# Performance work log

Hardware: AMD Instinct MI355X
Metric: run time of the kernel (lower is better)

## Reference

```python
import jax, jax.numpy as jnp
import numpy as np

D = 64   # hidden dim (input_dim == hidden_dims[i] == 64)
L = 6    # GNN layers per NBFNet
EPS = 1e-5

def _layer_norm(x, g, b):
    m = jnp.mean(x, axis=-1, keepdims=True)
    v = jnp.var(x, axis=-1, keepdims=True)
    return (x - m) * jax.lax.rsqrt(v + EPS) * g + b

def _conv(x, boundary, relation, edge_index, edge_type, W, b, g, bt):
    # GeneralizedRelationalConv: distmult message, sum aggregation with
    # boundary self-loop message, linear([input, agg]) -> LayerNorm -> ReLU.
    src, dst = edge_index[0], edge_index[1]
    msg = x[:, src, :] * relation[:, edge_type, :]                # [B,E,D]
    agg = boundary + jnp.zeros_like(x).at[:, dst, :].add(msg)     # edge_weight == 1
    out = jnp.einsum('bnf,fo->bno', jnp.concatenate([x, agg], axis=-1), W) + b
    return jax.nn.relu(_layer_norm(out, g, bt))

def _rel_model(q_rel, rel_edge_index, rel_edge_type, num_rel_nodes,
               rel_emb, Wr, br, gr, btr):
    # RelNBFNet.bellmanford: query = ones, boundary scatter at query relation node.
    B = q_rel.shape[0]
    query = jnp.ones((B, D), dtype=rel_emb.dtype)
    boundary = jnp.zeros((B, num_rel_nodes, D), rel_emb.dtype).at[jnp.arange(B), q_rel].add(query)
    relation = jnp.broadcast_to(rel_emb[None], (B,) + rel_emb.shape)  # dependent=False embedding
    def step(x, p):
        W, b, g, bt = p
        h = _conv(x, boundary, relation, rel_edge_index, rel_edge_type, W, b, g, bt)
        return h + x, None  # short_cut residual
    x, _ = jax.lax.scan(step, boundary, (Wr, br, gr, btr))
    return x  # [B, R, D]  (concat_hidden=False -> hiddens[-1])

def _ent_model(rel_repr, h_index, r_index, t_index, edge_index, edge_type,
               num_nodes, Wp1, bp1, Wp2, bp2, We, be, ge, bte, W1, b1, W2, b2):
    B = h_index.shape[0]
    query = rel_repr[jnp.arange(B), r_index]                      # [B,D]
    boundary = jnp.zeros((B, num_nodes, D), query.dtype).at[jnp.arange(B), h_index].add(query)
    def step(x, p):
        wp1, b1p, wp2, b2p, W, b, g, bt = p
        # project_relations=True: per-layer 2-layer MLP on relation representations
        rel = jax.nn.relu(rel_repr @ wp1 + b1p) @ wp2 + b2p       # [B,R,D]
        h = _conv(x, boundary, rel, edge_index, edge_type, W, b, g, bt)
        return h + x, None
    x, _ = jax.lax.scan(step, boundary, (Wp1, bp1, Wp2, bp2, We, be, ge, bte))
    node_query = jnp.broadcast_to(query[:, None, :], x.shape)
    feat = jnp.concatenate([x, node_query], axis=-1)              # [B,N,2D]
    feat = feat[jnp.arange(B)[:, None], t_index]                  # gather tails [B,K,2D]
    h = jax.nn.relu(feat @ W1 + b1)                               # num_mlp_layers=2
    return (h @ W2 + b2)[..., 0]                                  # [B,K]

def setup_inputs() -> dict:
    key = jax.random.key(0)
    ks = jax.random.split(key, 16)
    B, K, N, E, R, Er = 4, 256, 20000, 200000, 200, 4000
    ND = 100  # direct relations; R = 2*ND
    h = jax.random.randint(ks[0], (B,), 0, N)
    r = jax.random.randint(ks[1], (B,), 0, ND)
    t = jax.random.randint(ks[2], (B, K), 0, N)
    batch = jnp.stack([jnp.broadcast_to(h[:, None], (B, K)), t,
                       jnp.broadcast_to(r[:, None], (B, K))], axis=-1)
    s = 0.05
    return dict(
        batch=batch,
        edge_index=jax.random.randint(ks[3], (2, E), 0, N),
        edge_type=jax.random.randint(ks[4], (E,), 0, R),
        rel_edge_index=jax.random.randint(ks[5], (2, Er), 0, R),
        rel_edge_type=jax.random.randint(ks[6], (Er,), 0, 4),
        num_nodes=N, num_rel_nodes=R,
        rel_emb=jax.random.normal(ks[7], (4, D)) * s,
        Wr=jax.random.normal(ks[8], (L, 2 * D, D)) * s,
        br=jnp.zeros((L, D)), gr=jnp.ones((L, D)), btr=jnp.zeros((L, D)),
        Wp1=jax.random.normal(ks[9], (L, D, D)) * s,
        bp1=jnp.zeros((L, D)),
        Wp2=jax.random.normal(ks[10], (L, D, D)) * s,
        bp2=jnp.zeros((L, D)),
        We=jax.random.normal(ks[11], (L, 2 * D, D)) * s,
        be=jnp.zeros((L, D)), ge=jnp.ones((L, D)), bte=jnp.zeros((L, D)),
        W1=jax.random.normal(ks[12], (2 * D, 2 * D)) * s,
        b1=jnp.zeros((2 * D,)),
        W2=jax.random.normal(ks[13], (2 * D, 1)) * s,
        b2=jnp.zeros((1,)),
    )

def reference(batch, edge_index, edge_type, rel_edge_index, rel_edge_type,
              num_nodes, num_rel_nodes,
              rel_emb, Wr, br, gr, btr,
              Wp1, bp1, Wp2, bp2, We, be, ge, bte, W1, b1, W2, b2):
    # batch holds tail-negative triples (h, t, r) with constant h and r per row,
    # so negative_sample_to_tail is the identity here (eval mode: no edge removal).
    h_index = batch[:, 0, 0]
    t_index = batch[:, :, 1]
    r_index = batch[:, 0, 2]
    rel_repr = _rel_model(r_index, rel_edge_index, rel_edge_type, num_rel_nodes,
                          rel_emb, Wr, br, gr, btr)
    return _ent_model(rel_repr, h_index, r_index, t_index, edge_index, edge_type,
                      num_nodes, Wp1, bp1, Wp2, bp2, We, be, ge, bte, W1, b1, W2, b2)
```

## Files before the change

kernel.cpp:

```cpp
#include <hip/hip_runtime.h>
#include <hip/hip_bf16.h>

#define D_   64
#define L_   6
#define B_   4
#define K_   256
#define NN   20000
#define EE   200000
#define RR   200
#define ER_  4000
#define EPS_ 1e-5f

typedef unsigned short u16;
typedef unsigned int   u32;
typedef short bf16x8 __attribute__((ext_vector_type(8)));
typedef float f32x4  __attribute__((ext_vector_type(4)));

__device__ __forceinline__ u16 f2bf(float f) {
    u32 u = __float_as_uint(f);
    u += 0x7FFF + ((u >> 16) & 1);
    return (u16)(u >> 16);
}
__device__ __forceinline__ u32 pack2bf(float a, float b) {
    return (u32)f2bf(a) | ((u32)f2bf(b) << 16);
}
__device__ __forceinline__ float bflo(u32 u) { return __uint_as_float(u << 16); }
__device__ __forceinline__ float bfhi(u32 u) { return __uint_as_float(u & 0xFFFF0000u); }

__global__ __launch_bounds__(256)
void k_zero2(int* __restrict__ ec, int* __restrict__ rc) {
    int i = blockIdx.x * 256 + threadIdx.x;
    if (i < NN) ec[i] = 0;
    else if (i < NN + RR) rc[i - NN] = 0;
}

__global__ __launch_bounds__(256)
void k_hist2(const int* __restrict__ ei, const int* __restrict__ rei,
             int* __restrict__ ec, int* __restrict__ rc) {
    int g = blockIdx.x * 256 + threadIdx.x;
    if (g < EE) atomicAdd(&ec[ei[EE + g]], 1);
    else if (g < EE + ER_) atomicAdd(&rc[rei[ER_ + (g - EE)]], 1);
}

__global__ __launch_bounds__(256)
void k_scan1_2(const int* __restrict__ e_counts, int* __restrict__ e_pre, int* __restrict__ e_bs,
               const int* __restrict__ r_counts, int* __restrict__ r_pre, int* __restrict__ r_bs,
               int ent_nb) {
    __shared__ int tsum[256];
    const int* counts; int* pre; int* bs; int n; int blk;
    if ((int)blockIdx.x < ent_nb) { counts = e_counts; pre = e_pre; bs = e_bs; n = NN; blk = blockIdx.x; }
    else                          { counts = r_counts; pre = r_pre; bs = r_bs; n = RR; blk = 0; }
    int tid = threadIdx.x;
    int base = blk * 1024 + tid * 4;
    int c0 = 0, c1 = 0, c2 = 0, c3 = 0;
    if (base + 0 < n) c0 = counts[base + 0];
    if (base + 1 < n) c1 = counts[base + 1];
    if (base + 2 < n) c2 = counts[base + 2];
    if (base + 3 < n) c3 = counts[base + 3];
    tsum[tid] = c0 + c1 + c2 + c3;
    __syncthreads();
    if (tid == 0) {
        int acc = 0;
        for (int i = 0; i < 256; i++) { int t = tsum[i]; tsum[i] = acc; acc += t; }
    }
    __syncthreads();
    int run = tsum[tid];
    if (base + 0 < n) pre[base + 0] = run; run += c0;
    if (base + 1 < n) pre[base + 1] = run; run += c1;
    if (base + 2 < n) pre[base + 2] = run; run += c2;
    if (base + 3 < n) pre[base + 3] = run; run += c3;
    if (tid == 255) bs[blk] = run;
}

__global__ __launch_bounds__(64)
void k_scan2_2(int* __restrict__ eb, int enb, int* __restrict__ etot,
               int* __restrict__ rb, int rnb, int* __restrict__ rtot) {
    if (threadIdx.x == 0) {
        int acc = 0;
        for (int i = 0; i < enb; i++) { int t = eb[i]; eb[i] = acc; acc += t; }
        *etot = acc;
    }
    if (threadIdx.x == 1) {
        int acc = 0;
        for (int i = 0; i < rnb; i++) { int t = rb[i]; rb[i] = acc; acc += t; }
        *rtot = acc;
    }
}

__global__ __launch_bounds__(256)
void k_scan3_2(int* __restrict__ e_rp, const int* __restrict__ e_bs, int* __restrict__ e_cur,
               int* __restrict__ r_rp, const int* __restrict__ r_bs, int* __restrict__ r_cur) {
    int i = blockIdx.x * 256 + threadIdx.x;
    if (i < NN) {
        int v = e_rp[i] + e_bs[i >> 10];
        e_rp[i] = v; e_cur[i] = v;
    } else if (i < NN + RR) {
        int j = i - NN;
        int v = r_rp[j] + r_bs[j >> 10];
        r_rp[j] = v; r_cur[j] = v;
    }
}

__global__ __launch_bounds__(256)
void k_fill2(const int* __restrict__ ei, const int* __restrict__ et,
             const int* __restrict__ rei, const int* __restrict__ ret,
             int* __restrict__ e_cur, int* __restrict__ r_cur,
             int* __restrict__ e_packed, int* __restrict__ r_packed) {
    int g = blockIdx.x * 256 + threadIdx.x;
    if (g < EE) {
        int pos = atomicAdd(&e_cur[ei[EE + g]], 1);
        e_packed[pos] = ei[g] | (et[g] << 15);
    } else if (g < EE + ER_) {
        int h = g - EE;
        int pos = atomicAdd(&r_cur[rei[ER_ + h]], 1);
        r_packed[pos] = rei[h] | (ret[h] << 15);
    }
}

template<int NNODES, int MODE, bool FIRST>
__global__ __launch_bounds__(256)
void k_layer9(const float* __restrict__ xin, float* __restrict__ xout,
              const u16* __restrict__ xbin, u16* __restrict__ xbout,
              const void* __restrict__ relv,
              const int* __restrict__ rowptr, const int* __restrict__ packed,
              const float* __restrict__ query, const int* __restrict__ batch,
              const float* __restrict__ W, const float* __restrict__ bias,
              const float* __restrict__ gw, const float* __restrict__ bt) {
    __shared__ u16 Wt[64][72];
    __shared__ u16 As[16][72];
    __shared__ u16 Xs[16][72];
    __shared__ float LNbuf[16][68];
    const int tid   = threadIdx.x;
    const int node0 = blockIdx.x * 4;
    const int lane  = tid & 63;
    const int wv    = tid >> 6;

    int bn0 = batch[0 * K_ * 3 + (MODE ? 0 : 2)];
    int bn1 = batch[1 * K_ * 3 + (MODE ? 0 : 2)];
    int bn2 = batch[2 * K_ * 3 + (MODE ? 0 : 2)];
    int bn3 = batch[3 * K_ * 3 + (MODE ? 0 : 2)];

    const int gnode = node0 + wv;
    int beg = 0, end = 0;
    if (gnode < NNODES) { beg = rowptr[gnode]; end = rowptr[gnode + 1]; }

    const int erow  = wv * 4 + (lane >> 4);
    const int tx    = lane & 15;
    float4 resf = make_float4(0.f, 0.f, 0.f, 0.f);
    if constexpr (!FIRST) {
        int b = erow >> 2, nd = node0 + (erow & 3);
        if (nd < NNODES)
            resf = *reinterpret_cast<const float4*>(
                xin + ((size_t)b * NNODES + nd) * 64 + tx * 4);
    }

    {
        int n = lane, k16 = wv * 16;
        u32 buf[8];
        #pragma unroll
        for (int j2 = 0; j2 < 8; j2++) {
            float w0 = W[(64 + k16 + 2 * j2    ) * 64 + n];
            float w1 = W[(64 + k16 + 2 * j2 + 1) * 64 + n];
            buf[j2] = pack2bf(w0, w1);
        }
        uint4* dst = reinterpret_cast<uint4*>(&Wt[n][k16]);
        dst[0] = make_uint4(buf[0], buf[1], buf[2], buf[3]);
        dst[1] = make_uint4(buf[4], buf[5], buf[6], buf[7]);
    }

    if (tid < 128) {
        int m = tid >> 3, o8 = (tid & 7) * 8;
        int b = m >> 2, node = node0 + (m & 3);
        uint4 v = make_uint4(0, 0, 0, 0);
        if (node < NNODES) {
            if constexpr (FIRST) {
                int bnb = (b==0)?bn0:(b==1)?bn1:(b==2)?bn2:bn3;
                if (node == bnb) {
                    if constexpr (MODE == 1) {
                        const float* q = query + b * 64 + o8;
                        v = make_uint4(pack2bf(q[0], q[1]), pack2bf(q[2], q[3]),
                                       pack2bf(q[4], q[5]), pack2bf(q[6], q[7]));
                    } else {
                        v = make_uint4(0x3F803F80u, 0x3F803F80u, 0x3F803F80u, 0x3F803F80u);
                    }
                }
            } else if constexpr (MODE == 1) {
                v = *reinterpret_cast<const uint4*>(
                    xbin + ((size_t)b * NNODES + node) * 64 + o8);
            } else {
                const float* src = xin + ((size_t)b * NNODES + node) * 64 + o8;
                float4 x0 = *reinterpret_cast<const float4*>(src);
                float4 x1 = *reinterpret_cast<const float4*>(src + 4);
                v = make_uint4(pack2bf(x0.x, x0.y), pack2bf(x0.z, x0.w),
                               pack2bf(x1.x, x1.y), pack2bf(x1.z, x1.w));
            }
        }
        *reinterpret_cast<uint4*>(&Xs[m][o8]) = v;
    }

    const int slot = lane >> 3;
    const int d8   = lane & 7;

    float qreg[4][8];
    if constexpr (MODE == 1) {
        #pragma unroll
        for (int b = 0; b < 4; b++) {
            float4 q0 = *reinterpret_cast<const float4*>(query + b * 64 + d8 * 8);
            float4 q1 = *reinterpret_cast<const float4*>(query + b * 64 + d8 * 8 + 4);
            qreg[b][0]=q0.x; qreg[b][1]=q0.y; qreg[b][2]=q0.z; qreg[b][3]=q0.w;
            qreg[b][4]=q1.x; qreg[b][5]=q1.y; qreg[b][6]=q1.z; qreg[b][7]=q1.w;
        }
    }

    {
        float acc[4][8];
        #pragma unroll
        for (int b = 0; b < 4; b++)
            #pragma unroll
            for (int i = 0; i < 8; i++) acc[b][i] = 0.f;

        for (int e0 = beg; e0 < end; e0 += 16) {
            #pragma unroll
            for (int half = 0; half < 2; half++) {
                int e = e0 + half * 8 + slot;
                if (e < end) {
                    int p = packed[e];
                    int src = p & 0x7FFF;
                    int et  = p >> 15;
                    if constexpr (MODE == 1) {
                        const u16* rb = (const u16*)relv;
                        if constexpr (FIRST) {
                            #pragma unroll
                            for (int b = 0; b < 4; b++) {
                                int bnb = (b==0)?bn0:(b==1)?bn1:(b==2)?bn2:bn3;
                                if (src == bnb) {
                                    uint4 rv = *reinterpret_cast<const uint4*>(
                                        rb + ((size_t)(b * RR + et)) * 64 + d8 * 8);
                                    acc[b][0] = fmaf(qreg[b][0], bflo(rv.x), acc[b][0]);
                                    acc[b][1] = fmaf(qreg[b][1], bfhi(rv.x), acc[b][1]);
                                    acc[b][2] = fmaf(qreg[b][2], bflo(rv.y), acc[b][2]);
                                    acc[b][3] = fmaf(qreg[b][3], bfhi(rv.y), acc[b][3]);
                                    acc[b][4] = fmaf(qreg[b][4], bflo(rv.z), acc[b][4]);
                                    acc[b][5] = fmaf(qreg[b][5], bfhi(rv.z), acc[b][5]);
                                    acc[b][6] = fmaf(qreg[b][6], bflo(rv.w), acc[b][6]);
                                    acc[b][7] = fmaf(qreg[b][7], bfhi(rv.w), acc[b][7]);
                                }
                            }
                        } else {
                            #pragma unroll
                            for (int b = 0; b < 4; b++) {
                                uint4 xv = *reinterpret_cast<const uint4*>(
                                    xbin + ((size_t)(b * NNODES + src)) * 64 + d8 * 8);
                                uint4 rv = *reinterpret_cast<const uint4*>(
                                    ((const u16*)relv) + ((size_t)(b * RR + et)) * 64 + d8 * 8);
                                acc[b][0] = fmaf(bflo(xv.x), bflo(rv.x), acc[b][0]);
                                acc[b][1] = fmaf(bfhi(xv.x), bfhi(rv.x), acc[b][1]);
                                acc[b][2] = fmaf(bflo(xv.y), bflo(rv.y), acc[b][2]);
                                acc[b][3] = fmaf(bfhi(xv.y), bfhi(rv.y), acc[b][3]);
                                acc[b][4] = fmaf(bflo(xv.z), bflo(rv.z), acc[b][4]);
                                acc[b][5] = fmaf(bfhi(xv.z), bfhi(rv.z), acc[b][5]);
                                acc[b][6] = fmaf(bflo(xv.w), bflo(rv.w), acc[b][6]);
                                acc[b][7] = fmaf(bfhi(xv.w), bfhi(rv.w), acc[b][7]);
                            }
                        }
                    } else {
                        const float* re = (const float*)relv;
                        if constexpr (FIRST) {
                            bool m0 = (src == bn0), m1 = (src == bn1),
                                 m2 = (src == bn2), m3 = (src == bn3);
                            if (m0 | m1 | m2 | m3) {
                                float4 r0 = *reinterpret_cast<const float4*>(re + et * 64 + d8 * 8);
                                float4 r1 = *reinterpret_cast<const float4*>(re + et * 64 + d8 * 8 + 4);
                                float rr[8] = {r0.x,r0.y,r0.z,r0.w,r1.x,r1.y,r1.z,r1.w};
                                if (m0) {
                                    #pragma unroll
                                    for (int i = 0; i < 8; i++) acc[0][i] += rr[i];
                                }
                                if (m1) {
                                    #pragma unroll
                                    for (int i = 0; i < 8; i++) acc[1][i] += rr[i];
                                }
                                if (m2) {
                                    #pragma unroll
                                    for (int i = 0; i < 8; i++) acc[2][i] += rr[i];
                                }
                                if (m3) {
                                    #pragma unroll
                                    for (int i = 0; i < 8; i++) acc[3][i] += rr[i];
                                }
                            }
                        } else {
                            float4 r0 = *reinterpret_cast<const float4*>(re + et * 64 + d8 * 8);
                            float4 r1 = *reinterpret_cast<const float4*>(re + et * 64 + d8 * 8 + 4);
                            #pragma unroll
                            for (int b = 0; b < 4; b++) {
                                const float* xr = xin + ((size_t)(b * NNODES + src)) * 64 + d8 * 8;
                                float4 x0 = *reinterpret_cast<const float4*>(xr);
                                float4 x1 = *reinterpret_cast<const float4*>(xr + 4);
                                acc[b][0] = fmaf(x0.x, r0.x, acc[b][0]);
                                acc[b][1] = fmaf(x0.y, r0.y, acc[b][1]);
                                acc[b][2] = fmaf(x0.z, r0.z, acc[b][2]);
                                acc[b][3] = fmaf(x0.w, r0.w, acc[b][3]);
                                acc[b][4] = fmaf(x1.x, r1.x, acc[b][4]);
                                acc[b][5] = fmaf(x1.y, r1.y, acc[b][5]);
                                acc[b][6] = fmaf(x1.z, r1.z, acc[b][6]);
                                acc[b][7] = fmaf(x1.w, r1.w, acc[b][7]);
                            }
                        }
                    }
                }
            }
        }

        #pragma unroll
        for (int b = 0; b < 4; b++)
            #pragma unroll
            for (int i = 0; i < 8; i++) {
                float v = acc[b][i];
                v += __shfl_xor(v, 8);
                v += __shfl_xor(v, 16);
                v += __shfl_xor(v, 32);
                acc[b][i] = v;
            }

        if (slot < 4) {
            float out[8];
            #pragma unroll
            for (int i = 0; i < 8; i++)
                out[i] = (slot==0) ? acc[0][i] : (slot==1) ? acc[1][i]
                       : (slot==2) ? acc[2][i] : acc[3][i];
            int bnb = (slot==0)?bn0:(slot==1)?bn1:(slot==2)?bn2:bn3;
            if (gnode < NNODES && gnode == bnb) {
                if constexpr (MODE == 1) {
                    #pragma unroll
                    for (int i = 0; i < 8; i++)
                        out[i] += (slot==0)?qreg[0][i]:(slot==1)?qreg[1][i]
                                 :(slot==2)?qreg[2][i]:qreg[3][i];
                } else {
                    #pragma unroll
                    for (int i = 0; i < 8; i++) out[i] += 1.0f;
                }
            }
            int m = slot * 4 + wv;
            *reinterpret_cast<uint4*>(&As[m][d8 * 8]) =
                make_uint4(pack2bf(out[0], out[1]), pack2bf(out[2], out[3]),
                           pack2bf(out[4], out[5]), pack2bf(out[6], out[7]));
        }
    }
    __syncthreads();

    const int al = lane & 15;
    const int ag = lane >> 4;
    const int nt = wv;
    f32x4 acc4 = (f32x4){0.f, 0.f, 0.f, 0.f};
    {
        bf16x8 a0 = *reinterpret_cast<const bf16x8*>(&As[al][ag * 8]);
        bf16x8 a1 = *reinterpret_cast<const bf16x8*>(&As[al][32 + ag * 8]);
        bf16x8 b0 = *reinterpret_cast<const bf16x8*>(&Wt[nt * 16 + al][ag * 8]);
        bf16x8 b1 = *reinterpret_cast<const bf16x8*>(&Wt[nt * 16 + al][32 + ag * 8]);
        acc4 = __builtin_amdgcn_mfma_f32_16x16x32_bf16(a0, b0, acc4, 0, 0, 0);
        acc4 = __builtin_amdgcn_mfma_f32_16x16x32_bf16(a1, b1, acc4, 0, 0, 0);
    }
    __syncthreads();

    {
        int n = lane, k16 = wv * 16;
        u32 buf[8];
        #pragma unroll
        for (int j2 = 0; j2 < 8; j2++) {
            float w0 = W[(k16 + 2 * j2    ) * 64 + n];
            float w1 = W[(k16 + 2 * j2 + 1) * 64 + n];
            buf[j2] = pack2bf(w0, w1);
        }
        uint4* dst = reinterpret_cast<uint4*>(&Wt[n][k16]);
        dst[0] = make_uint4(buf[0], buf[1], buf[2], buf[3]);
        dst[1] = make_uint4(buf[4], buf[5], buf[6], buf[7]);
    }
    __syncthreads();

    {
        bf16x8 x0 = *reinterpret_cast<const bf16x8*>(&Xs[al][ag * 8]);
        bf16x8 x1 = *reinterpret_cast<const bf16x8*>(&Xs[al][32 + ag * 8]);
        bf16x8 b0 = *reinterpret_cast<const bf16x8*>(&Wt[nt * 16 + al][ag * 8]);
        bf16x8 b1 = *reinterpret_cast<const bf16x8*>(&Wt[nt * 16 + al][32 + ag * 8]);
        acc4 = __builtin_amdgcn_mfma_f32_16x16x32_bf16(x0, b0, acc4, 0, 0, 0);
        acc4 = __builtin_amdgcn_mfma_f32_16x16x32_bf16(x1, b1, acc4, 0, 0, 0);
    }
    #pragma unroll
    for (int reg = 0; reg < 4; reg++)
        LNbuf[ag * 4 + reg][nt * 16 + al] = acc4[reg];
    __syncthreads();

    {
        int row = erow;
        int b = row >> 2, node = node0 + (row & 3);
        float o[4];
        float s1 = 0.f, s2 = 0.f;
        #pragma unroll
        for (int i = 0; i < 4; i++) {
            o[i] = LNbuf[row][tx * 4 + i] + bias[tx * 4 + i];
            s1 += o[i];
            s2 += o[i] * o[i];
        }
        s1 += __shfl_xor(s1, 1); s2 += __shfl_xor(s2, 1);
        s1 += __shfl_xor(s1, 2); s2 += __shfl_xor(s2, 2);
        s1 += __shfl_xor(s1, 4); s2 += __shfl_xor(s2, 4);
        s1 += __shfl_xor(s1, 8); s2 += __shfl_xor(s2, 8);
        float mean = s1 * (1.f / 64.f);
        float var  = s2 * (1.f / 64.f) - mean * mean;
        float inv  = rsqrtf(var + EPS_);
        if (node < NNODES) {
            int bnb = (b==0)?bn0:(b==1)?bn1:(b==2)?bn2:bn3;
            size_t ro = ((size_t)b * NNODES + node) * 64;
            float r[4] = {resf.x, resf.y, resf.z, resf.w};
            if constexpr (FIRST) {
                r[0] = r[1] = r[2] = r[3] = 0.f;
                if (node == bnb) {
                    if constexpr (MODE == 1) {
                        float4 q = *reinterpret_cast<const float4*>(query + b * 64 + tx * 4);
                        r[0] = q.x; r[1] = q.y; r[2] = q.z; r[3] = q.w;
                    } else {
                        r[0] = r[1] = r[2] = r[3] = 1.0f;
                    }
                }
            }
            float nv[4];
            #pragma unroll
            for (int i = 0; i < 4; i++) {
                float h = (o[i] - mean) * inv * gw[tx * 4 + i] + bt[tx * 4 + i];
                h = fmaxf(h, 0.f);
                nv[i] = r[i] + h;
            }
            *reinterpret_cast<float4*>(&xout[ro + tx * 4]) =
                make_float4(nv[0], nv[1], nv[2], nv[3]);
            if constexpr (MODE == 1) {
                ushort4 b4;
                b4.x = f2bf(nv[0]); b4.y = f2bf(nv[1]);
                b4.z = f2bf(nv[2]); b4.w = f2bf(nv[3]);
                *reinterpret_cast<ushort4*>(&xbout[ro + tx * 4]) = b4;
            }
        }
    }
}

__global__ __launch_bounds__(64)
void k_rel_mlp_all(const float* __restrict__ rel_repr,
                   const float* __restrict__ Wp1, const float* __restrict__ bp1,
                   const float* __restrict__ Wp2, const float* __restrict__ bp2,
                   u16* __restrict__ out) {
    __shared__ float rowv[64];
    __shared__ float hid[64];
    int l     = blockIdx.x / (B_ * RR);
    int rowid = blockIdx.x % (B_ * RR);
    int d = threadIdx.x;
    const float* w1 = Wp1 + l * 4096;
    const float* w2 = Wp2 + l * 4096;
    rowv[d] = rel_repr[rowid * 64 + d];
    __syncthreads();
    float acc = bp1[l * 64 + d];
    for (int k = 0; k < 64; k++) acc = fmaf(rowv[k], w1[k * 64 + d], acc);
    hid[d] = fmaxf(acc, 0.f);
    __syncthreads();
    float o = bp2[l * 64 + d];
    for (int k = 0; k < 64; k++) o = fmaf(hid[k], w2[k * 64 + d], o);
    out[(size_t)l * B_ * RR * 64 + rowid * 64 + d] = f2bf(o);
}

__global__ __launch_bounds__(256)
void k_query(const float* __restrict__ rel_repr, const int* __restrict__ batch,
             float* __restrict__ query) {
    int tid = threadIdx.x;
    int b = tid >> 6;
    int d = tid & 63;
    int r = batch[b * K_ * 3 + 2];
    query[b * 64 + d] = rel_repr[(b * RR + r) * 64 + d];
}

__global__ __launch_bounds__(128)
void k_final(const float* __restrict__ x, const float* __restrict__ query,
             const int* __restrict__ batch,
             const float* __restrict__ W1, const float* __restrict__ b1,
             const float* __restrict__ W2, const float* __restrict__ b2,
             float* __restrict__ out) {
    __shared__ float feat[128];
    __shared__ float partial[2];
    int pair = blockIdx.x;
    int b = pair / K_;
    int t = batch[pair * 3 + 1];
    int d = threadIdx.x;
    feat[d] = (d < 64) ? x[(size_t)(b * NN + t) * 64 + d] : query[b * 64 + (d - 64)];
    __syncthreads();
    float h = b1[d];
    for (int i = 0; i < 128; i++) h = fmaf(feat[i], W1[i * 128 + d], h);
    h = fmaxf(h, 0.f);
    float v = h * W2[d];
    #pragma unroll
    for (int off = 1; off < 64; off <<= 1) v += __shfl_xor(v, off);
    if ((d & 63) == 0) partial[d >> 6] = v;
    __syncthreads();
    if (d == 0) out[pair] = partial[0] + partial[1] + b2[0];
}

extern "C" void kernel_launch(void* const* d_in, const int* in_sizes, int n_in,
                              void* d_out, int out_size, void* d_ws, size_t ws_size,
                              hipStream_t stream) {
    const int* batch      = (const int*)d_in[0];
    const int* edge_index = (const int*)d_in[1];
    const int* edge_type  = (const int*)d_in[2];
    const int* rel_ei     = (const int*)d_in[3];
    const int* rel_et     = (const int*)d_in[4];
    const float* rel_emb = (const float*)d_in[7];
    const float* Wr  = (const float*)d_in[8];
    const float* br  = (const float*)d_in[9];
    const float* gr  = (const float*)d_in[10];
    const float* btr = (const float*)d_in[11];
    const float* Wp1 = (const float*)d_in[12];
    const float* bp1 = (const float*)d_in[13];
    const float* Wp2 = (const float*)d_in[14];
    const float* bp2 = (const float*)d_in[15];
    const float* We  = (const float*)d_in[16];
    const float* be  = (const float*)d_in[17];
    const float* ge  = (const float*)d_in[18];
    const float* bte = (const float*)d_in[19];
    const float* W1  = (const float*)d_in[20];
    const float* b1  = (const float*)d_in[21];
    const float* W2  = (const float*)d_in[22];
    const float* b2  = (const float*)d_in[23];

    float* ws = (float*)d_ws;
    float* rel_buf0 = ws;
    float* rel_buf1 = rel_buf0 + 51200;
    float* query    = rel_buf1 + 51200;
    float* x0       = query + 256;
    float* x1       = x0 + (size_t)B_ * NN * 64;
    u16*   xb0      = (u16*)(x1 + (size_t)B_ * NN * 64);
    u16*   xb1      = xb0 + (size_t)B_ * NN * 64;
    u16*   rel_all  = xb1 + (size_t)B_ * NN * 64;
    int*   iw       = (int*)(rel_all + (size_t)L_ * B_ * RR * 64);

    int* ent_counts  = iw;
    int* ent_rowptr  = ent_counts + NN;
    int* ent_bsums   = ent_rowptr + NN + 1;
    int* ent_packed  = ent_bsums + 32;
    int* rel_counts  = ent_packed + EE;
    int* rel_rowptr  = rel_counts + RR;
    int* rel_bsums   = rel_rowptr + RR + 1;
    int* rel_packed  = rel_bsums + 8;

    const int ENT_NB = (NN + 1023) / 1024;
    const int REL_NB = (RR + 1023) / 1024;

    k_zero2<<<(NN + RR + 255) / 256, 256, 0, stream>>>(ent_counts, rel_counts);
    k_hist2<<<(EE + ER_ + 255) / 256, 256, 0, stream>>>(edge_index, rel_ei, ent_counts, rel_counts);
    k_scan1_2<<<ENT_NB + REL_NB, 256, 0, stream>>>(ent_counts, ent_rowptr, ent_bsums,
                                                   rel_counts, rel_rowptr, rel_bsums, ENT_NB);
    k_scan2_2<<<1, 64, 0, stream>>>(ent_bsums, ENT_NB, ent_rowptr + NN,
                                    rel_bsums, REL_NB, rel_rowptr + RR);
    k_scan3_2<<<(NN + RR + 255) / 256, 256, 0, stream>>>(ent_rowptr, ent_bsums, ent_counts,
                                                         rel_rowptr, rel_bsums, rel_counts);
    k_fill2<<<(EE + ER_ + 255) / 256, 256, 0, stream>>>(edge_index, edge_type, rel_ei, rel_et,
                                                        ent_counts, rel_counts, ent_packed, rel_packed);

    float* rf[2] = {rel_buf0, rel_buf1};
    const int RGRID = (RR + 3) / 4;
    k_layer9<RR, 0, true><<<RGRID, 256, 0, stream>>>(
        nullptr, rf[0], nullptr, nullptr, rel_emb,
        rel_rowptr, rel_packed, nullptr, batch,
        Wr, br, gr, btr);
    int rc = 0;
    for (int l = 1; l < L_; ++l) {
        k_layer9<RR, 0, false><<<RGRID, 256, 0, stream>>>(
            rf[rc], rf[rc ^ 1], nullptr, nullptr, rel_emb,
            rel_rowptr, rel_packed, nullptr, batch,
            Wr + l * 8192, br + l * 64, gr + l * 64, btr + l * 64);
        rc ^= 1;
    }
    float* rel_final = rf[rc];

    k_query<<<1, 256, 0, stream>>>(rel_final, batch, query);
    k_rel_mlp_all<<<L_ * B_ * RR, 64, 0, stream>>>(rel_final, Wp1, bp1, Wp2, bp2, rel_all);
    float* xf[2] = {x0, x1};
    u16*   xh[2] = {xb0, xb1};
    const int EGRID = (NN + 3) / 4;
    k_layer9<NN, 1, true><<<EGRID, 256, 0, stream>>>(
        nullptr, xf[0], nullptr, xh[0], rel_all,
        ent_rowptr, ent_packed, query, batch,
        We, be, ge, bte);
    int ec = 0;
    for (int l = 1; l < L_; ++l) {
        k_layer9<NN, 1, false><<<EGRID, 256, 0, stream>>>(
            xf[ec], xf[ec ^ 1], xh[ec], xh[ec ^ 1],
            rel_all + (size_t)l * B_ * RR * 64,
            ent_rowptr, ent_packed, query, batch,
            We + l * 8192, be + l * 64, ge + l * 64, bte + l * 64);
        ec ^= 1;
    }
    k_final<<<B_ * K_, 128, 0, stream>>>(xf[ec], query, batch, W1, b1, W2, b2,
                                         (float*)d_out);
}
```

Baseline: 400.7 us.

## Make layer kernel persistent with grid-stride tiles and hoisted bf16 weights

The layer kernel becomes persistent: each block converts and stages both halves of the 128x64 weight matrix in LDS once, then loops over 4-node tiles in grid-stride fashion. The entity layers launch a fixed 1536 blocks instead of one block per tile, and launch bounds request 6 blocks per CU. This removes the per-tile global weight reload, bf16 conversion and the extra barriers between the two GEMM halves. In exchange it uses more LDS per block, may lower occupancy or constrain registers, and can leave load imbalance across the fixed grid.

Measured after the change: 692.0 us. 1.73x slower.

```diff
diff --git a/kernel.cpp b/kernel.cpp
--- a/kernel.cpp
+++ b/kernel.cpp
@@ -118,20 +118,20 @@
 }
 
 template<int NNODES, int MODE, bool FIRST>
-__global__ __launch_bounds__(256)
-void k_layer9(const float* __restrict__ xin, float* __restrict__ xout,
-              const u16* __restrict__ xbin, u16* __restrict__ xbout,
-              const void* __restrict__ relv,
-              const int* __restrict__ rowptr, const int* __restrict__ packed,
-              const float* __restrict__ query, const int* __restrict__ batch,
-              const float* __restrict__ W, const float* __restrict__ bias,
-              const float* __restrict__ gw, const float* __restrict__ bt) {
-    __shared__ u16 Wt[64][72];
+__global__ __launch_bounds__(256, 6)
+void k_layer10(const float* __restrict__ xin, float* __restrict__ xout,
+               const u16* __restrict__ xbin, u16* __restrict__ xbout,
+               const void* __restrict__ relv,
+               const int* __restrict__ rowptr, const int* __restrict__ packed,
+               const float* __restrict__ query, const int* __restrict__ batch,
+               const float* __restrict__ W, const float* __restrict__ bias,
+               const float* __restrict__ gw, const float* __restrict__ bt,
+               int ntiles) {
+    __shared__ u16 Wt[2][64][72];
     __shared__ u16 As[16][72];
     __shared__ u16 Xs[16][72];
-    __shared__ float LNbuf[16][68];
+    __shared__ float LNbuf[16][65];
     const int tid   = threadIdx.x;
-    const int node0 = blockIdx.x * 4;
     const int lane  = tid & 63;
     const int wv    = tid >> 6;
 
@@ -140,68 +140,24 @@
     int bn2 = batch[2 * K_ * 3 + (MODE ? 0 : 2)];
     int bn3 = batch[3 * K_ * 3 + (MODE ? 0 : 2)];
 
-    const int gnode = node0 + wv;
-    int beg = 0, end = 0;
-    if (gnode < NNODES) { beg = rowptr[gnode]; end = rowptr[gnode + 1]; }
-
-    const int erow  = wv * 4 + (lane >> 4);
-    const int tx    = lane & 15;
-    float4 resf = make_float4(0.f, 0.f, 0.f, 0.f);
-    if constexpr (!FIRST) {
-        int b = erow >> 2, nd = node0 + (erow & 3);
-        if (nd < NNODES)
-            resf = *reinterpret_cast<const float4*>(
-                xin + ((size_t)b * NNODES + nd) * 64 + tx * 4);
-    }
-
-    {
+    #pragma unroll
+    for (int half = 0; half < 2; half++) {
         int n = lane, k16 = wv * 16;
         u32 buf[8];
         #pragma unroll
         for (int j2 = 0; j2 < 8; j2++) {
-            float w0 = W[(64 + k16 + 2 * j2    ) * 64 + n];
-            float w1 = W[(64 + k16 + 2 * j2 + 1) * 64 + n];
+            float w0 = W[(half * 64 + k16 + 2 * j2    ) * 64 + n];
+            float w1 = W[(half * 64 + k16 + 2 * j2 + 1) * 64 + n];
             buf[j2] = pack2bf(w0, w1);
         }
-        uint4* dst = reinterpret_cast<uint4*>(&Wt[n][k16]);
+        uint4* dst = reinterpret_cast<uint4*>(&Wt[half][n][k16]);
         dst[0] = make_uint4(buf[0], buf[1], buf[2], buf[3]);
         dst[1] = make_uint4(buf[4], buf[5], buf[6], buf[7]);
     }
 
-    if (tid < 128) {
-        int m = tid >> 3, o8 = (tid & 7) * 8;
-        int b = m >> 2, node = node0 + (m & 3);
-        uint4 v = make_uint4(0, 0, 0, 0);
-        if (node < NNODES) {
-            if constexpr (FIRST) {
-                int bnb = (b==0)?bn0:(b==1)?bn1:(b==2)?bn2:bn3;
-                if (node == bnb) {
-                    if constexpr (MODE == 1) {
-                        const float* q = query + b * 64 + o8;
-                        v = make_uint4(pack2bf(q[0], q[1]), pack2bf(q[2], q[3]),
-                                       pack2bf(q[4], q[5]), pack2bf(q[6], q[7]));
-                    } else {
-                        v = make_uint4(0x3F803F80u, 0x3F803F80u, 0x3F803F80u, 0x3F803F80u);
-                    }
-                }
-            } else if constexpr (MODE == 1) {
-                v = *reinterpret_cast<const uint4*>(
-                    xbin + ((size_t)b * NNODES + node) * 64 + o8);
-            } else {
-                const float* src = xin + ((size_t)b * NNODES + node) * 64 + o8;
-                float4 x0 = *reinterpret_cast<const float4*>(src);
-                float4 x1 = *reinterpret_cast<const float4*>(src + 4);
-                v = make_uint4(pack2bf(x0.x, x0.y), pack2bf(x0.z, x0.w),
-                               pack2bf(x1.x, x1.y), pack2bf(x1.z, x1.w));
-            }
-        }
-        *reinterpret_cast<uint4*>(&Xs[m][o8]) = v;
-    }
-
+    float qreg[4][8];
     const int slot = lane >> 3;
     const int d8   = lane & 7;
-
-    float qreg[4][8];
     if constexpr (MODE == 1) {
         #pragma unroll
         for (int b = 0; b < 4; b++) {
@@ -212,232 +168,262 @@
         }
     }
 
-    {
-        float acc[4][8];
-        #pragma unroll
-        for (int b = 0; b < 4; b++)
+    const int erow = wv * 4 + (lane >> 4);
+    const int tx   = lane & 15;
+    const int al   = lane & 15;
+    const int ag   = lane >> 4;
+
+    for (int tile = blockIdx.x; tile < ntiles; tile += gridDim.x) {
+        const int node0 = tile * 4;
+
+        const int gnode = node0 + wv;
+        int beg = 0, end = 0;
+        if (gnode < NNODES) { beg = rowptr[gnode]; end = rowptr[gnode + 1]; }
+
+        float4 resf = make_float4(0.f, 0.f, 0.f, 0.f);
+        if constexpr (!FIRST) {
+            int b = erow >> 2, nd = node0 + (erow & 3);
+            if (nd < NNODES)
+                resf = *reinterpret_cast<const float4*>(
+                    xin + ((size_t)b * NNODES + nd) * 64 + tx * 4);
+        }
+
+        if (tid < 128) {
+            int m = tid >> 3, o8 = (tid & 7) * 8;
+            int b = m >> 2, node = node0 + (m & 3);
+            uint4 v = make_uint4(0, 0, 0, 0);
+            if (node < NNODES) {
+                if constexpr (FIRST) {
+                    int bnb = (b==0)?bn0:(b==1)?bn1:(b==2)?bn2:bn3;
+                    if (node == bnb) {
+                        if constexpr (MODE == 1) {
+                            const float* q = query + b * 64 + o8;
+                            v = make_uint4(pack2bf(q[0], q[1]), pack2bf(q[2], q[3]),
+                                           pack2bf(q[4], q[5]), pack2bf(q[6], q[7]));
+                        } else {
+                            v = make_uint4(0x3F803F80u, 0x3F803F80u, 0x3F803F80u, 0x3F803F80u);
+                        }
+                    }
+                } else if constexpr (MODE == 1) {
+                    v = *reinterpret_cast<const uint4*>(
+                        xbin + ((size_t)b * NNODES + node) * 64 + o8);
+                } else {
+                    const float* src = xin + ((size_t)b * NNODES + node) * 64 + o8;
+                    float4 x0 = *reinterpret_cast<const float4*>(src);
+                    float4 x1 = *reinterpret_cast<const float4*>(src + 4);
+                    v = make_uint4(pack2bf(x0.x, x0.y), pack2bf(x0.z, x0.w),
+                                   pack2bf(x1.x, x1.y), pack2bf(x1.z, x1.w));
+                }
+            }
+            *reinterpret_cast<uint4*>(&Xs[m][o8]) = v;
+        }
+
+        {
+            float acc[4][8];
             #pragma unroll
-            for (int i = 0; i < 8; i++) acc[b][i] = 0.f;
-
-        for (int e0 = beg; e0 < end; e0 += 16) {
-            #pragma unroll
-            for (int half = 0; half < 2; half++) {
-                int e = e0 + half * 8 + slot;
-                if (e < end) {
-                    int p = packed[e];
-                    int src = p & 0x7FFF;
-                    int et  = p >> 15;
-                    if constexpr (MODE == 1) {
-                        const u16* rb = (const u16*)relv;
-                        if constexpr (FIRST) {
-                            #pragma unroll
-                            for (int b = 0; b < 4; b++) {
-                                int bnb = (b==0)?bn0:(b==1)?bn1:(b==2)?bn2:bn3;
-                                if (src == bnb) {
+            for (int b = 0; b < 4; b++)
+                #pragma unroll
+                for (int i = 0; i < 8; i++) acc[b][i] = 0.f;
+
+            for (int e0 = beg; e0 < end; e0 += 16) {
+                #pragma unroll
+                for (int half = 0; half < 2; half++) {
+                    int e = e0 + half * 8 + slot;
+                    if (e < end) {
+                        int p = packed[e];
+                        int src = p & 0x7FFF;
+                        int et  = p >> 15;
+                        if constexpr (MODE == 1) {
+                            const u16* rb = (const u16*)relv;
+                            if constexpr (FIRST) {
+                                #pragma unroll
+                                for (int b = 0; b < 4; b++) {
+                                    int bnb = (b==0)?bn0:(b==1)?bn1:(b==2)?bn2:bn3;
+                                    if (src == bnb) {
+                                        uint4 rv = *reinterpret_cast<const uint4*>(
+                                            rb + ((size_t)(b * RR + et)) * 64 + d8 * 8);
+                                        acc[b][0] = fmaf(qreg[b][0], bflo(rv.x), acc[b][0]);
+                                        acc[b][1] = fmaf(qreg[b][1], bfhi(rv.x), acc[b][1]);
+                                        acc[b][2] = fmaf(qreg[b][2], bflo(rv.y), acc[b][2]);
+                                        acc[b][3] = fmaf(qreg[b][3], bfhi(rv.y), acc[b][3]);
+                                        acc[b][4] = fmaf(qreg[b][4], bflo(rv.z), acc[b][4]);
+                                        acc[b][5] = fmaf(qreg[b][5], bfhi(rv.z), acc[b][5]);
+                                        acc[b][6] = fmaf(qreg[b][6], bflo(rv.w), acc[b][6]);
+                                        acc[b][7] = fmaf(qreg[b][7], bfhi(rv.w), acc[b][7]);
+                                    }
+                                }
+                            } else {
+                                #pragma unroll
+                                for (int b = 0; b < 4; b++) {
+                                    uint4 xv = *reinterpret_cast<const uint4*>(
+                                        xbin + ((size_t)(b * NNODES + src)) * 64 + d8 * 8);
                                     uint4 rv = *reinterpret_cast<const uint4*>(
-                                        rb + ((size_t)(b * RR + et)) * 64 + d8 * 8);
-                                    acc[b][0] = fmaf(qreg[b][0], bflo(rv.x), acc[b][0]);
-                                    acc[b][1] = fmaf(qreg[b][1], bfhi(rv.x), acc[b][1]);
-                                    acc[b][2] = fmaf(qreg[b][2], bflo(rv.y), acc[b][2]);
-                                    acc[b][3] = fmaf(qreg[b][3], bfhi(rv.y), acc[b][3]);
-                                    acc[b][4] = fmaf(qreg[b][4], bflo(rv.z), acc[b][4]);
-                                    acc[b][5] = fmaf(qreg[b][5], bfhi(rv.z), acc[b][5]);
-                                    acc[b][6] = fmaf(qreg[b][6], bflo(rv.w), acc[b][6]);
-                                    acc[b][7] = fmaf(qreg[b][7], bfhi(rv.w), acc[b][7]);
+                                        ((const u16*)relv) + ((size_t)(b * RR + et)) * 64 + d8 * 8);
+                                    acc[b][0] = fmaf(bflo(xv.x), bflo(rv.x), acc[b][0]);
+                                    acc[b][1] = fmaf(bfhi(xv.x), bfhi(rv.x), acc[b][1]);
+                                    acc[b][2] = fmaf(bflo(xv.y), bflo(rv.y), acc[b][2]);
+                                    acc[b][3] = fmaf(bfhi(xv.y), bfhi(rv.y), acc[b][3]);
+                                    acc[b][4] = fmaf(bflo(xv.z), bflo(rv.z), acc[b][4]);
+                                    acc[b][5] = fmaf(bfhi(xv.z), bfhi(rv.z), acc[b][5]);
+                                    acc[b][6] = fmaf(bflo(xv.w), bflo(rv.w), acc[b][6]);
+                                    acc[b][7] = fmaf(bfhi(xv.w), bfhi(rv.w), acc[b][7]);
                                 }
                             }
                         } else {
-                            #pragma unroll
-                            for (int b = 0; b < 4; b++) {
-                                uint4 xv = *reinterpret_cast<const uint4*>(
-                                    xbin + ((size_t)(b * NNODES + src)) * 64 + d8 * 8);
-                                uint4 rv = *reinterpret_cast<const uint4*>(
-                                    ((const u16*)relv) + ((size_t)(b * RR + et)) * 64 + d8 * 8);
-                                acc[b][0] = fmaf(bflo(xv.x), bflo(rv.x), acc[b][0]);
-                                acc[b][1] = fmaf(bfhi(xv.x), bfhi(rv.x), acc[b][1]);
-                                acc[b][2] = fmaf(bflo(xv.y), bflo(rv.y), acc[b][2]);
-                                acc[b][3] = fmaf(bfhi(xv.y), bfhi(rv.y), acc[b][3]);
-                                acc[b][4] = fmaf(bflo(xv.z), bflo(rv.z), acc[b][4]);
-                                acc[b][5] = fmaf(bfhi(xv.z), bfhi(rv.z), acc[b][5]);
-                                acc[b][6] = fmaf(bflo(xv.w), bflo(rv.w), acc[b][6]);
-                                acc[b][7] = fmaf(bfhi(xv.w), bfhi(rv.w), acc[b][7]);
-                            }
-                        }
-                    } else {
-                        const float* re = (const float*)relv;
-                        if constexpr (FIRST) {
-                            bool m0 = (src == bn0), m1 = (src == bn1),
-                                 m2 = (src == bn2), m3 = (src == bn3);
-                            if (m0 | m1 | m2 | m3) {
+                            const float* re = (const float*)relv;
+                            if constexpr (FIRST) {
+                                bool m0 = (src == bn0), m1 = (src == bn1),
+                                     m2 = (src == bn2), m3 = (src == bn3);
+                                if (m0 | m1 | m2 | m3) {
+                                    float4 r0 = *reinterpret_cast<const float4*>(re + et * 64 + d8 * 8);
+                                    float4 r1 = *reinterpret_cast<const float4*>(re + et * 64 + d8 * 8 + 4);
+                                    float rr[8] = {r0.x,r0.y,r0.z,r0.w,r1.x,r1.y,r1.z,r1.w};
+                                    if (m0) {
+                                        #pragma unroll
+                                        for (int i = 0; i < 8; i++) acc[0][i] += rr[i];
+                                    }
+                                    if (m1) {
+                                        #pragma unroll
+                                        for (int i = 0; i < 8; i++) acc[1][i] += rr[i];
+                                    }
+                                    if (m2) {
+                                        #pragma unroll
+                                        for (int i = 0; i < 8; i++) acc[2][i] += rr[i];
+                                    }
+                                    if (m3) {
+                                        #pragma unroll
+                                        for (int i = 0; i < 8; i++) acc[3][i] += rr[i];
+                                    }
+                                }
+                            } else {
                                 float4 r0 = *reinterpret_cast<const float4*>(re + et * 64 + d8 * 8);
                                 float4 r1 = *reinterpret_cast<const float4*>(re + et * 64 + d8 * 8 + 4);
-                                float rr[8] = {r0.x,r0.y,r0.z,r0.w,r1.x,r1.y,r1.z,r1.w};
-                                if (m0) {
-                                    #pragma unroll
-                                    for (int i = 0; i < 8; i++) acc[0][i] += rr[i];
+                                #pragma unroll
+                                for (int b = 0; b < 4; b++) {
+                                    const float* xr = xin + ((size_t)(b * NNODES + src)) * 64 + d8 * 8;
+                                    float4 x0 = *reinterpret_cast<const float4*>(xr);
+                                    float4 x1 = *reinterpret_cast<const float4*>(xr + 4);
+                                    acc[b][0] = fmaf(x0.x, r0.x, acc[b][0]);
+                                    acc[b][1] = fmaf(x0.y, r0.y, acc[b][1]);
+                                    acc[b][2] = fmaf(x0.z, r0.z, acc[b][2]);
+                                    acc[b][3] = fmaf(x0.w, r0.w, acc[b][3]);
+                                    acc[b][4] = fmaf(x1.x, r1.x, acc[b][4]);
+                                    acc[b][5] = fmaf(x1.y, r1.y, acc[b][5]);
+                                    acc[b][6] = fmaf(x1.z, r1.z, acc[b][6]);
+                                    acc[b][7] = fmaf(x1.w, r1.w, acc[b][7]);
                                 }
-                                if (m1) {
-                                    #pragma unroll
-                                    for (int i = 0; i < 8; i++) acc[1][i] += rr[i];
-                                }
-                                if (m2) {
-                                    #pragma unroll
-                                    for (int i = 0; i < 8; i++) acc[2][i] += rr[i];
-                                }
-                                if (m3) {
-                                    #pragma unroll
-                                    for (int i = 0; i < 8; i++) acc[3][i] += rr[i];
-                                }
-                            }
-                        } else {
-                            float4 r0 = *reinterpret_cast<const float4*>(re + et * 64 + d8 * 8);
-                            float4 r1 = *reinterpret_cast<const float4*>(re + et * 64 + d8 * 8 + 4);
-                            #pragma unroll
-                            for (int b = 0; b < 4; b++) {
-                                const float* xr = xin + ((size_t)(b * NNODES + src)) * 64 + d8 * 8;
-                                float4 x0 = *reinterpret_cast<const float4*>(xr);
-                                float4 x1 = *reinterpret_cast<const float4*>(xr + 4);
-                                acc[b][0] = fmaf(x0.x, r0.x, acc[b][0]);
-                                acc[b][1] = fmaf(x0.y, r0.y, acc[b][1]);
-                                acc[b][2] = fmaf(x0.z, r0.z, acc[b][2]);
-                                acc[b][3] = fmaf(x0.w, r0.w, acc[b][3]);
-                                acc[b][4] = fmaf(x1.x, r1.x, acc[b][4]);
-                                acc[b][5] = fmaf(x1.y, r1.y, acc[b][5]);
-                                acc[b][6] = fmaf(x1.z, r1.z, acc[b][6]);
-                                acc[b][7] = fmaf(x1.w, r1.w, acc[b][7]);
                             }
                         }
                     }
                 }
             }
-        }
-
+
+            #pragma unroll
+            for (int b = 0; b < 4; b++)
+                #pragma unroll
+                for (int i = 0; i < 8; i++) {
+                    float v = acc[b][i];
+                    v += __shfl_xor(v, 8);
+                    v += __shfl_xor(v, 16);
+                    v += __shfl_xor(v, 32);
+                    acc[b][i] = v;
+                }
+
+            if (slot < 4) {
+                float out[8];
+                #pragma unroll
+                for (int i = 0; i < 8; i++)
+                    out[i] = (slot==0) ? acc[0][i] : (slot==1) ? acc[1][i]
+                           : (slot==2) ? acc[2][i] : acc[3][i];
+                int bnb = (slot==0)?bn0:(slot==1)?bn1:(slot==2)?bn2:bn3;
+                if (gnode < NNODES && gnode == bnb) {
+                    if constexpr (MODE == 1) {
+                        #pragma unroll
+                        for (int i = 0; i < 8; i++)
+                            out[i] += (slot==0)?qreg[0][i]:(slot==1)?qreg[1][i]
+                                     :(slot==2)?qreg[2][i]:qreg[3][i];
+                    } else {
+                        #pragma unroll
+                        for (int i = 0; i < 8; i++) out[i] += 1.0f;
+                    }
+                }
+                int m = slot * 4 + wv;
+                *reinterpret_cast<uint4*>(&As[m][d8 * 8]) =
+                    make_uint4(pack2bf(out[0], out[1]), pack2bf(out[2], out[3]),
+                               pack2bf(out[4], out[5]), pack2bf(out[6], out[7]));
+            }
+        }
+        __syncthreads();
+
+        const int nt = wv;
+        f32x4 acc4 = (f32x4){0.f, 0.f, 0.f, 0.f};
+        {
+            bf16x8 a0 = *reinterpret_cast<const bf16x8*>(&As[al][ag * 8]);
+            bf16x8 a1 = *reinterpret_cast<const bf16x8*>(&As[al][32 + ag * 8]);
+            bf16x8 b0 = *reinterpret_cast<const bf16x8*>(&Wt[1][nt * 16 + al][ag * 8]);
+            bf16x8 b1 = *reinterpret_cast<const bf16x8*>(&Wt[1][nt * 16 + al][32 + ag * 8]);
+            acc4 = __builtin_amdgcn_mfma_f32_16x16x32_bf16(a0, b0, acc4, 0, 0, 0);
+            acc4 = __builtin_amdgcn_mfma_f32_16x16x32_bf16(a1, b1, acc4, 0, 0, 0);
+            bf16x8 x0 = *reinterpret_cast<const bf16x8*>(&Xs[al][ag * 8]);
+            bf16x8 x1 = *reinterpret_cast<const bf16x8*>(&Xs[al][32 + ag * 8]);
+            bf16x8 d0 = *reinterpret_cast<const bf16x8*>(&Wt[0][nt * 16 + al][ag * 8]);
+            bf16x8 d1 = *reinterpret_cast<const bf16x8*>(&Wt[0][nt * 16 + al][32 + ag * 8]);
+            acc4 = __builtin_amdgcn_mfma_f32_16x16x32_bf16(x0, d0, acc4, 0, 0, 0);
+            acc4 = __builtin_amdgcn_mfma_f32_16x16x32_bf16(x1, d1, acc4, 0, 0, 0);
+        }
         #pragma unroll
-        for (int b = 0; b < 4; b++)
-            #pragma unroll
-            for (int i = 0; i < 8; i++) {
-                float v = acc[b][i];
-                v += __shfl_xor(v, 8);
-                v += __shfl_xor(v, 16);
-                v += __shfl_xor(v, 32);
-                acc[b][i] = v;
-            }
-
-        if (slot < 4) {
-            float out[8];
-            #pragma unroll
-            for (int i = 0; i < 8; i++)
-                out[i] = (slot==0) ? acc[0][i] : (slot==1) ? acc[1][i]
-                       : (slot==2) ? acc[2][i] : acc[3][i];
-            int bnb = (slot==0)?bn0:(slot==1)?bn1:(slot==2)?bn2:bn3;
-            if (gnode < NNODES && gnode == bnb) {
-                if constexpr (MODE == 1) {
-                    #pragma unroll
-                    for (int i = 0; i < 8; i++)
-                        out[i] += (slot==0)?qreg[0][i]:(slot==1)?qreg[1][i]
-                                 :(slot==2)?qreg[2][i]:qreg[3][i];
-                } else {
-                    #pragma unroll
-                    for (int i = 0; i < 8; i++) out[i] += 1.0f;
-                }
-            }
-            int m = slot * 4 + wv;
-            *reinterpret_cast<uint4*>(&As[m][d8 * 8]) =
-                make_uint4(pack2bf(out[0], out[1]), pack2bf(out[2], out[3]),
-                           pack2bf(out[4], out[5]), pack2bf(out[6], out[7]));
-        }
-    }
-    __syncthreads();
-
-    const int al = lane & 15;
-    const int ag = lane >> 4;
-    const int nt = wv;
-    f32x4 acc4 = (f32x4){0.f, 0.f, 0.f, 0.f};
-    {
-        bf16x8 a0 = *reinterpret_cast<const bf16x8*>(&As[al][ag * 8]);
-        bf16x8 a1 = *reinterpret_cast<const bf16x8*>(&As[al][32 + ag * 8]);
-        bf16x8 b0 = *reinterpret_cast<const bf16x8*>(&Wt[nt * 16 + al][ag * 8]);
-        bf16x8 b1 = *reinterpret_cast<const bf16x8*>(&Wt[nt * 16 + al][32 + ag * 8]);
-        acc4 = __builtin_amdgcn_mfma_f32_16x16x32_bf16(a0, b0, acc4, 0, 0, 0);
-        acc4 = __builtin_amdgcn_mfma_f32_16x16x32_bf16(a1, b1, acc4, 0, 0, 0);
-    }
-    __syncthreads();
-
-    {
-        int n = lane, k16 = wv * 16;
-        u32 buf[8];
-        #pragma unroll
-        for (int j2 = 0; j2 < 8; j2++) {
-            float w0 = W[(k16 + 2 * j2    ) * 64 + n];
-            float w1 = W[(k16 + 2 * j2 + 1) * 64 + n];
-            buf[j2] = pack2bf(w0, w1);
-        }
-        uint4* dst = reinterpret_cast<uint4*>(&Wt[n][k16]);
-        dst[0] = make_uint4(buf[0], buf[1], buf[2], buf[3]);
-        dst[1] = make_uint4(buf[4], buf[5], buf[6], buf[7]);
-    }
-    __syncthreads();
-
-    {
-        bf16x8 x0 = *reinterpret_cast<const bf16x8*>(&Xs[al][ag * 8]);
-        bf16x8 x1 = *reinterpret_cast<const bf16x8*>(&Xs[al][32 + ag * 8]);
-        bf16x8 b0 = *reinterpret_cast<const bf16x8*>(&Wt[nt * 16 + al][ag * 8]);
-        bf16x8 b1 = *reinterpret_cast<const bf16x8*>(&Wt[nt * 16 + al][32 + ag * 8]);
-        acc4 = __builtin_amdgcn_mfma_f32_16x16x32_bf16(x0, b0, acc4, 0, 0, 0);
-        acc4 = __builtin_amdgcn_mfma_f32_16x16x32_bf16(x1, b1, acc4, 0, 0, 0);
-    }
-    #pragma unroll
-    for (int reg = 0; reg < 4; reg++)
-        LNbuf[ag * 4 + reg][nt * 16 + al] = acc4[reg];
-    __syncthreads();
-
-    {
-        int row = erow;
-        int b = row >> 2, node = node0 + (row & 3);
-        float o[4];
-        float s1 = 0.f, s2 = 0.f;
-        #pragma unroll
-        for (int i = 0; i < 4; i++) {
-            o[i] = LNbuf[row][tx * 4 + i] + bias[tx * 4 + i];
-            s1 += o[i];
-            s2 += o[i] * o[i];
-        }
-        s1 += __shfl_xor(s1, 1); s2 += __shfl_xor(s2, 1);
-        s1 += __shfl_xor(s1, 2); s2 += __shfl_xor(s2, 2);
-        s1 += __shfl_xor(s1, 4); s2 += __shfl_xor(s2, 4);
-        s1 += __shfl_xor(s1, 8); s2 += __shfl_xor(s2, 8);
-        float mean = s1 * (1.f / 64.f);
-        float var  = s2 * (1.f / 64.f) - mean * mean;
-        float inv  = rsqrtf(var + EPS_);
-        if (node < NNODES) {
-            int bnb = (b==0)?bn0:(b==1)?bn1:(b==2)?bn2:bn3;
-            size_t ro = ((size_t)b * NNODES + node) * 64;
-            float r[4] = {resf.x, resf.y, resf.z, resf.w};
-            if constexpr (FIRST) {
-                r[0] = r[1] = r[2] = r[3] = 0.f;
-                if (node == bnb) {
-                    if constexpr (MODE == 1) {
-                        float4 q = *reinterpret_cast<const float4*>(query + b * 64 + tx * 4);
-                        r[0] = q.x; r[1] = q.y; r[2] = q.z; r[3] = q.w;
-                    } else {
-                        r[0] = r[1] = r[2] = r[3] = 1.0f;
-                    }
-                }
-            }
-            float nv[4];
+        for (int reg = 0; reg < 4; reg++)
+            LNbuf[ag * 4 + reg][nt * 16 + al] = acc4[reg];
+        __syncthreads();
+
+        {
+            int row = erow;
+            int b = row >> 2, node = node0 + (row & 3);
+            float o[4];
+            float s1 = 0.f, s2 = 0.f;
             #pragma unroll
             for (int i = 0; i < 4; i++) {
-                float h = (o[i] - mean) * inv * gw[tx * 4 + i] + bt[tx * 4 + i];
-                h = fmaxf(h, 0.f);
-                nv[i] = r[i] + h;
+                o[i] = LNbuf[row][tx * 4 + i] + bias[tx * 4 + i];
+                s1 += o[i];
+                s2 += o[i] * o[i];
             }
-            *reinterpret_cast<float4*>(&xout[ro + tx * 4]) =
-                make_float4(nv[0], nv[1], nv[2], nv[3]);
-            if constexpr (MODE == 1) {
-                ushort4 b4;
-                b4.x = f2bf(nv[0]); b4.y = f2bf(nv[1]);
-                b4.z = f2bf(nv[2]); b4.w = f2bf(nv[3]);
-                *reinterpret_cast<ushort4*>(&xbout[ro + tx * 4]) = b4;
+            s1 += __shfl_xor(s1, 1); s2 += __shfl_xor(s2, 1);
+            s1 += __shfl_xor(s1, 2); s2 += __shfl_xor(s2, 2);
+            s1 += __shfl_xor(s1, 4); s2 += __shfl_xor(s2, 4);
+            s1 += __shfl_xor(s1, 8); s2 += __shfl_xor(s2, 8);
+            float mean = s1 * (1.f / 64.f);
+            float var  = s2 * (1.f / 64.f) - mean * mean;
+            float inv  = rsqrtf(var + EPS_);
+            if (node < NNODES) {
+                int bnb = (b==0)?bn0:(b==1)?bn1:(b==2)?bn2:bn3;
+                size_t ro = ((size_t)b * NNODES + node) * 64;
+                float r[4] = {resf.x, resf.y, resf.z, resf.w};
+                if constexpr (FIRST) {
+                    r[0] = r[1] = r[2] = r[3] = 0.f;
+                    if (node == bnb) {
+                        if constexpr (MODE == 1) {
+                            float4 q = *reinterpret_cast<const float4*>(query + b * 64 + tx * 4);
+                            r[0] = q.x; r[1] = q.y; r[2] = q.z; r[3] = q.w;
+                        } else {
+                            r[0] = r[1] = r[2] = r[3] = 1.0f;
+                        }
+                    }
+                }
+                float nv[4];
+                #pragma unroll
+                for (int i = 0; i < 4; i++) {
+                    float h = (o[i] - mean) * inv * gw[tx * 4 + i] + bt[tx * 4 + i];
+                    h = fmaxf(h, 0.f);
+                    nv[i] = r[i] + h;
+                }
+                *reinterpret_cast<float4*>(&xout[ro + tx * 4]) =
+                    make_float4(nv[0], nv[1], nv[2], nv[3]);
+                if constexpr (MODE == 1) {
+                    ushort4 b4;
+                    b4.x = f2bf(nv[0]); b4.y = f2bf(nv[1]);
+                    b4.z = f2bf(nv[2]); b4.w = f2bf(nv[3]);
+                    *reinterpret_cast<ushort4*>(&xbout[ro + tx * 4]) = b4;
+                }
             }
         }
     }
@@ -562,17 +548,17 @@
                                                         ent_counts, rel_counts, ent_packed, rel_packed);
 
     float* rf[2] = {rel_buf0, rel_buf1};
-    const int RGRID = (RR + 3) / 4;
-    k_layer9<RR, 0, true><<<RGRID, 256, 0, stream>>>(
+    const int RTILES = (RR + 3) / 4;
+    k_layer10<RR, 0, true><<<RTILES, 256, 0, stream>>>(
         nullptr, rf[0], nullptr, nullptr, rel_emb,
         rel_rowptr, rel_packed, nullptr, batch,
-        Wr, br, gr, btr);
+        Wr, br, gr, btr, RTILES);
     int rc = 0;
     for (int l = 1; l < L_; ++l) {
-        k_layer9<RR, 0, false><<<RGRID, 256, 0, stream>>>(
+        k_layer10<RR, 0, false><<<RTILES, 256, 0, stream>>>(
             rf[rc], rf[rc ^ 1], nullptr, nullptr, rel_emb,
             rel_rowptr, rel_packed, nullptr, batch,
-            Wr + l * 8192, br + l * 64, gr + l * 64, btr + l * 64);
+            Wr + l * 8192, br + l * 64, gr + l * 64, btr + l * 64, RTILES);
         rc ^= 1;
     }
     float* rel_final = rf[rc];
@@ -581,18 +567,19 @@
     k_rel_mlp_all<<<L_ * B_ * RR, 64, 0, stream>>>(rel_final, Wp1, bp1, Wp2, bp2, rel_all);
     float* xf[2] = {x0, x1};
     u16*   xh[2] = {xb0, xb1};
-    const int EGRID = (NN + 3) / 4;
-    k_layer9<NN, 1, true><<<EGRID, 256, 0, stream>>>(
+    const int ETILES = (NN + 3) / 4;
+    const int EGRID  = 1536;
+    k_layer10<NN, 1, true><<<EGRID, 256, 0, stream>>>(
         nullptr, xf[0], nullptr, xh[0], rel_all,
         ent_rowptr, ent_packed, query, batch,
-        We, be, ge, bte);
+        We, be, ge, bte, ETILES);
     int ec = 0;
     for (int l = 1; l < L_; ++l) {
-        k_layer9<NN, 1, false><<<EGRID, 256, 0, stream>>>(
+        k_layer10<NN, 1, false><<<EGRID, 256, 0, stream>>>(
             xf[ec], xf[ec ^ 1], xh[ec], xh[ec ^ 1],
             rel_all + (size_t)l * B_ * RR * 64,
             ent_rowptr, ent_packed, query, batch,
-            We + l * 8192, be + l * 64, ge + l * 64, bte + l * 64);
+            We + l * 8192, be + l * 64, ge + l * 64, bte + l * 64, ETILES);
         ec ^= 1;
     }
     k_final<<<B_ * K_, 128, 0, stream>>>(xf[ec], query, batch, W1, b1, W2, b2,
```
